# Kernel optimization log

Measured on AMD Instinct MI355X. Metric: run time of the kernel, lower is better.

The kernel has to match this reference:

```python
import jax, jax.numpy as jnp
import numpy as np

V = 20000   # token vocab (num_embeddings)
SC = 4000   # sub-char vocab (new_size of sub_char embedding)
D = 128     # embedding_dim
L = 15      # max nodes per decomposition tree (<= 8 leaves)
B, S = 32, 512


def _build_trees(rng):
    """Random binary decomposition trees in topological order (children < parent)."""
    node_ids = np.zeros((V, L), np.int32)
    left = np.full((V, L), -1, np.int32)
    right = np.full((V, L), -1, np.int32)
    last = np.zeros((V,), np.int32)
    for v in range(V):
        n_leaves = int(rng.integers(2, 9))
        stack, nodes = [], []
        leaves_left = n_leaves
        while leaves_left > 0 or len(stack) > 1:
            if leaves_left > 0 and (len(stack) < 2 or rng.random() < 0.5):
                nodes.append((-1, -1)); leaves_left -= 1
            else:
                r = stack.pop(); l = stack.pop()
                nodes.append((l, r))
            stack.append(len(nodes) - 1)
        n = len(nodes)
        for j, (l, r) in enumerate(nodes):
            left[v, j] = l; right[v, j] = r
        node_ids[v, :n] = rng.integers(0, SC, n)
        last[v] = n - 1
    return node_ids, left, right, last


def setup_inputs() -> dict:
    key = jax.random.key(0)
    k1, k2, k3, k4 = jax.random.split(key, 4)
    rng = np.random.default_rng(0)
    node_ids, left, right, last = _build_trees(rng)
    inp = {
        "input": jax.random.randint(k1, (B, S), 0, V, dtype=jnp.int32),
        "node_ids": jnp.asarray(node_ids),
        "left": jnp.asarray(left),
        "right": jnp.asarray(right),
        "last": jnp.asarray(last),
        "emb": jax.random.normal(k2, (SC, 5 * D), jnp.float32) * 0.1,   # sub_char weights
        "Wlh_w": jax.random.normal(k3, (D, 5 * D), jnp.float32) * 0.05,  # Linear(D,5D), x @ W
        "Wlh_b": jnp.zeros((5 * D,), jnp.float32),
        "Wrh_w": jax.random.normal(k4, (D, 5 * D), jnp.float32) * 0.05,
        "Wrh_b": jnp.zeros((5 * D,), jnp.float32),
    }
    return inp


def _tree_lstm(node_ids, left, right, last, emb, Wlh_w, Wlh_b, Wrh_w, Wrh_b):
    nV, nL = node_ids.shape
    gv = jnp.arange(nV)

    def step(carry, xs):
        h_all, c_all = carry                  # [V, L, D] each
        ids, l, r, j = xs                     # [V], [V], [V], scalar
        is_int = (l >= 0)[:, None]            # internal node mask; leaf has l==r==-1
        li, ri = jnp.maximum(l, 0), jnp.maximum(r, 0)
        hl, hr = h_all[gv, li], h_all[gv, ri]  # gather children states [V, D]
        cl, cr = c_all[gv, li], c_all[gv, ri]
        s = emb[ids]                           # [V, 5D]
        s_int = s + (hl @ Wlh_w + Wlh_b) + (hr @ Wrh_w + Wrh_b)
        s = jnp.where(is_int, s_int, s)
        ig, lfg, rfg, og, ug = jnp.split(s, 5, axis=1)
        c = jax.nn.sigmoid(ig) * jnp.tanh(ug)
        c = c + jnp.where(is_int, jax.nn.sigmoid(lfg) * cl + jax.nn.sigmoid(rfg) * cr, 0.0)
        h = jax.nn.sigmoid(og) * jnp.tanh(c)
        h_all = h_all.at[:, j].set(h)
        c_all = c_all.at[:, j].set(c)
        return (h_all, c_all), None

    init = (jnp.zeros((nV, nL, emb.shape[1] // 5), emb.dtype),
            jnp.zeros((nV, nL, emb.shape[1] // 5), emb.dtype))
    xs = (node_ids.T, left.T, right.T, jnp.arange(nL))
    (h_all, _), _ = jax.lax.scan(step, init, xs)
    return h_all[gv, last]                     # root h per vocab entry [V, D]


def reference(input, node_ids, left, right, last, emb, Wlh_w, Wlh_b, Wrh_w, Wrh_b):
    lut = _tree_lstm(node_ids, left, right, last, emb, Wlh_w, Wlh_b, Wrh_w, Wrh_b)  # [V, D]
    return lut[input]                          # [B, S, D]
```

## Files before the change

### kernel.cpp

```cpp
#include <hip/hip_runtime.h>
#include <hip/hip_fp16.h>
#include <math.h>

#define V    20000
#define SCV  4000
#define LL   15
#define OUTN (16384 * 128)

#define LEAF_BIT 0x40000000
#define REF_MASK 0x3FFFFFFF
#define ROOT_BIT 0x20000000
#define SLOT_MASK 0x1FFFFFFF
#define DUMMY_SLOT 89999

#define OFF_COUNTS 0
#define OFF_ROOT   128
#define OFF_LISTS  80384
#define OFF_LEAFC  5968384
#define OFF_LEAFHH 8016384
#define OFF_EMBT   9040384
#define OFF_WT     19280384
#define OFF_BIAS   19608064
#define OFF_HINT   19610624
#define OFF_CINT   65690624
#define OFF_HH     111770624
#define OFF_USED   134810624

__device__ __constant__ int d_listOff[8] = {0, 0, 80000, 120000, 160000, 180000, 200000, 220000};

#define MT 128

typedef _Float16 f16x8 __attribute__((ext_vector_type(8)));
typedef float    f32x4 __attribute__((ext_vector_type(4)));

__device__ __forceinline__ float sigm(float x) { return 1.0f / (1.0f + expf(-x)); }

__global__ void prep_kernel(const int* __restrict__ input,
                            const float* __restrict__ emb,
                            const float* __restrict__ Wl, const float* __restrict__ Wlb,
                            const float* __restrict__ Wr, const float* __restrict__ Wrb,
                            float* __restrict__ leafC, __half* __restrict__ leafHh,
                            __half* __restrict__ embT,
                            __half* __restrict__ WT, float* __restrict__ biasSum,
                            unsigned char* __restrict__ used) {
    __shared__ float T[64][65];
    int t = threadIdx.x, bid = blockIdx.x;
    for (int r = bid * 2 + (t >> 7); r < SCV; r += gridDim.x * 2) {
        int i = t & 127;
        const float* e = emb + r * 640;
        float c = sigm(e[i]) * tanhf(e[512 + i]);
        float h = sigm(e[384 + i]) * tanhf(c);
        leafC[r * 128 + i] = c;
        leafHh[r * 128 + i] = __float2half(h);
    }
    for (int idx = bid * 256 + t; idx < SCV * 128; idx += gridDim.x * 256) {
        int id = idx >> 7, dd = idx & 127;
        const float* e = emb + id * 640 + dd;
        __half v[8];
#pragma unroll
        for (int p = 0; p < 5; ++p) v[p] = __float2half(e[p * 128]);
        v[5] = __float2half(0.f); v[6] = v[5]; v[7] = v[5];
        *(uint4*)(embT + (size_t)idx * 8) = *(const uint4*)v;
    }
    for (int i = bid * 256 + t; i < 16384; i += gridDim.x * 256)
        used[input[i]] = 1;
    if (bid == 41)
        for (int i = t; i < 640; i += 256) biasSum[i] = Wlb[i] + Wrb[i];
    if (bid < 40) {
        int kb = (bid & 3) * 64, nb = (bid >> 2) * 64;
        int tx = t & 63, ty = t >> 6;
        for (int kk = ty; kk < 64; kk += 4) {
            int k = kb + kk;
            const float* Wsrc = (k < 128) ? (Wl + k * 640) : (Wr + (k - 128) * 640);
            T[kk][tx] = Wsrc[nb + tx];
        }
        __syncthreads();
        for (int nn = ty; nn < 64; nn += 4)
            WT[(nb + nn) * 256 + kb + tx] = __float2half(T[tx][nn]);
    }
}

__global__ void meta_kernel(const int* __restrict__ node_ids,
                            const int* __restrict__ left,
                            const int* __restrict__ right,
                            const int* __restrict__ last,
                            const unsigned char* __restrict__ used,
                            int* __restrict__ counts,
                            int* __restrict__ rootSlot,
                            int4* __restrict__ lists) {
    __shared__ int  sHei[MT][17];
    __shared__ int  sRef[MT][17];
    __shared__ int4 ebuf[MT][7];
    __shared__ int  ebin[MT][7];
    __shared__ int  locCnt[8];
    __shared__ int  basePos[8];
    __shared__ int  scanBuf[MT];
    __shared__ int  blockBase;

    int tid = threadIdx.x;
    if (tid < 8) locCnt[tid] = 0;
    __syncthreads();

    int v = blockIdx.x * MT + tid;
    int nInt = 0;
    if (v < V && used[v]) {
        int l15[LL], r15[LL], id15[LL];
#pragma unroll
        for (int j = 0; j < LL; ++j) {
            l15[j]  = left[v * LL + j];
            r15[j]  = right[v * LL + j];
            id15[j] = node_ids[v * LL + j];
        }
        int lastv = last[v];
#pragma unroll
        for (int j = 0; j < LL; ++j) {
            if (j <= lastv) {
                int l = l15[j];
                if (l < 0) {
                    sHei[tid][j] = 0;
                    sRef[tid][j] = LEAF_BIT | id15[j];
                } else {
                    int r = r15[j];
                    int hl = sHei[tid][l], hr = sHei[tid][r];
                    int hh = 1 + (hl > hr ? hl : hr);
                    sHei[tid][j] = hh;
                    int pos = atomicAdd(&locCnt[hh], 1);
                    int flag = (j == lastv) ? ROOT_BIT : 0;
                    ebuf[tid][nInt] = make_int4(nInt | flag, id15[j], sRef[tid][l], sRef[tid][r]);
                    ebin[tid][nInt] = (hh << 16) | pos;
                    sRef[tid][j] = nInt;
                    ++nInt;
                }
            }
        }
    }
    scanBuf[tid] = nInt;
    __syncthreads();
    for (int d = 1; d < MT; d <<= 1) {
        int val = (tid >= d) ? scanBuf[tid - d] : 0;
        __syncthreads();
        scanBuf[tid] += val;
        __syncthreads();
    }
    if (tid == 0) blockBase = atomicAdd(&counts[31], scanBuf[MT - 1]);
    if (tid < 8) {
        int c = locCnt[tid];
        basePos[tid] = c ? atomicAdd(&counts[tid], c) : 0;
    }
    __syncthreads();
    int treeBase = blockBase + scanBuf[tid] - nInt;
    if (v < V && nInt > 0) rootSlot[v] = treeBase + nInt - 1;
    for (int e = 0; e < nInt; ++e) {
        int4 E  = ebuf[tid][e];
        int md  = ebin[tid][e];
        int hh  = md >> 16, pos = md & 0xFFFF;
        E.x += treeBase;
        E.z = (E.z & LEAF_BIT) ? E.z : (E.z + treeBase);
        E.w = (E.w & LEAF_BIT) ? E.w : (E.w + treeBase);
        lists[d_listOff[hh] + basePos[hh] + pos] = E;
    }
}

__launch_bounds__(512, 4)
__global__ void round_mfma(const int4* __restrict__ list, const int* __restrict__ cntPtr,
                           const __half* __restrict__ embT, const __half* __restrict__ WT,
                           const float* __restrict__ biasSum,
                           const __half* __restrict__ leafHh, const float* __restrict__ leafC,
                           float* __restrict__ hInt, float* __restrict__ cInt,
                           __half* __restrict__ hH) {
    __shared__ __half Ah[32][264];
    __shared__ int4 meta[32];
    int cnt = *cntPtr;
    int nGroups = (cnt + 31) >> 5;
    int t = threadIdx.x;
    int lane = t & 63, wave = t >> 6;
    int ln15 = lane & 15, quad = lane >> 4;
    int d = 16 * wave + ln15;
    float bs[5];
#pragma unroll
    for (int p = 0; p < 5; ++p) bs[p] = biasSum[p * 128 + d];
    const __half* wbase = WT + d * 256 + quad * 8;

    for (int grp = blockIdx.x; grp < nGroups; grp += gridDim.x) {
        int base = grp * 32;
        int rows = cnt - base; if (rows > 32) rows = 32;
        if (t < 32) {
            int4 E;
            if (t < rows) E = list[base + t];
            else { E.x = DUMMY_SLOT; E.y = 0; E.z = LEAF_BIT; E.w = LEAF_BIT; }
            meta[t] = E;
        }
        __syncthreads();
#pragma unroll
        for (int it = 0; it < 2; ++it) {
            int idx = t + it * 512;
            int m = idx >> 5, q = idx & 31;
            int ref = (q < 16) ? meta[m].z : meta[m].w;
            const __half* hs = (ref & LEAF_BIT) ? leafHh : hH;
            uint4 v = *(const uint4*)(hs + (ref & REF_MASK) * 128 + (q & 15) * 8);
            *(uint4*)(&Ah[m][q * 8]) = v;
        }
        f32x4 acc[2][5];
#pragma unroll
        for (int c = 0; c < 2; ++c)
#pragma unroll
            for (int r = 0; r < 4; ++r) {
                int id = meta[c * 16 + quad * 4 + r].y;
                f16x8 ev = *(const f16x8*)((const void*)(embT + ((size_t)id * 128 + d) * 8));
#pragma unroll
                for (int p = 0; p < 5; ++p)
                    acc[c][p][r] = (float)ev[p] + bs[p];
            }
        __syncthreads();
#pragma unroll 2
        for (int kb = 0; kb < 8; ++kb) {
            f16x8 bf[5];
#pragma unroll
            for (int p = 0; p < 5; ++p)
                bf[p] = *(const f16x8*)((const void*)(wbase + p * 32768 + kb * 32));
            f16x8 af[2];
#pragma unroll
            for (int c = 0; c < 2; ++c)
                af[c] = *(const f16x8*)((const void*)&Ah[c * 16 + ln15][kb * 32 + quad * 8]);
#pragma unroll
            for (int p = 0; p < 5; ++p)
#pragma unroll
                for (int c = 0; c < 2; ++c)
                    acc[c][p] = __builtin_amdgcn_mfma_f32_16x16x32_f16(af[c], bf[p], acc[c][p], 0, 0, 0);
        }
#pragma unroll
        for (int c = 0; c < 2; ++c)
#pragma unroll
            for (int r = 0; r < 4; ++r) {
                int4 E = meta[c * 16 + quad * 4 + r];
                float ig = acc[c][0][r], lfg = acc[c][1][r], rfg = acc[c][2][r];
                float og = acc[c][3][r], ug = acc[c][4][r];
                float cl = ((E.z & LEAF_BIT) ? leafC : cInt)[(E.z & REF_MASK) * 128 + d];
                float cr = ((E.w & LEAF_BIT) ? leafC : cInt)[(E.w & REF_MASK) * 128 + d];
                float cc = sigm(ig) * tanhf(ug) + sigm(lfg) * cl + sigm(rfg) * cr;
                float hh2 = sigm(og) * tanhf(cc);
                int slot = E.x & SLOT_MASK;
                if (E.x & ROOT_BIT) {
                    hInt[slot * 128 + d] = hh2;
                } else {
                    cInt[slot * 128 + d] = cc;
                    hH[slot * 128 + d] = __float2half(hh2);
                }
            }
        __syncthreads();
    }
}

__global__ void gather_kernel(const int* __restrict__ input,
                              const int* __restrict__ rootSlot,
                              const float* __restrict__ hInt,
                              float4* __restrict__ out) {
    int idx = blockIdx.x * 256 + threadIdx.x;
    int token = input[idx >> 5];
    int d = idx & 31;
    out[idx] = ((const float4*)hInt)[rootSlot[token] * 32 + d];
}

extern "C" void kernel_launch(void* const* d_in, const int* in_sizes, int n_in,
                              void* d_out, int out_size, void* d_ws, size_t ws_size,
                              hipStream_t stream) {
    const int*   input    = (const int*)d_in[0];
    const int*   node_ids = (const int*)d_in[1];
    const int*   left     = (const int*)d_in[2];
    const int*   right    = (const int*)d_in[3];
    const int*   last     = (const int*)d_in[4];
    const float* emb      = (const float*)d_in[5];
    const float* Wl       = (const float*)d_in[6];
    const float* Wlb      = (const float*)d_in[7];
    const float* Wr       = (const float*)d_in[8];
    const float* Wrb      = (const float*)d_in[9];
    float* out = (float*)d_out;

    char* ws = (char*)d_ws;
    int*    counts   = (int*)(ws + OFF_COUNTS);
    int*    rootSlot = (int*)(ws + OFF_ROOT);
    int4*   lists    = (int4*)(ws + OFF_LISTS);
    float*  leafC    = (float*)(ws + OFF_LEAFC);
    __half* leafHh   = (__half*)(ws + OFF_LEAFHH);
    __half* embT     = (__half*)(ws + OFF_EMBT);
    __half* WT       = (__half*)(ws + OFF_WT);
    float*  biasSum  = (float*)(ws + OFF_BIAS);
    float*  hInt     = (float*)(ws + OFF_HINT);
    float*  cInt     = (float*)(ws + OFF_CINT);
    __half* hH       = (__half*)(ws + OFF_HH);
    unsigned char* usedp = (unsigned char*)(ws + OFF_USED);

    (void)hipMemsetAsync(counts, 0, 128, stream);
    (void)hipMemsetAsync(usedp, 0, V, stream);

    prep_kernel<<<1024, 256, 0, stream>>>(input, emb, Wl, Wlb, Wr, Wrb,
                                          leafC, leafHh, embT, WT, biasSum, usedp);
    meta_kernel<<<(V + MT - 1) / MT, MT, 0, stream>>>(node_ids, left, right, last, usedp,
                                                      counts, rootSlot, lists);

    static const int h_listOff[8] = {0, 0, 80000, 120000, 160000, 180000, 200000, 220000};
    static const int h_grid[8]    = {0, 1024, 512, 256, 128, 32, 16, 8};
    for (int h = 1; h <= 7; ++h) {
        round_mfma<<<h_grid[h], 512, 0, stream>>>(
            lists + h_listOff[h], counts + h,
            embT, WT, biasSum, leafHh, leafC, hInt, cInt, hH);
    }

    gather_kernel<<<OUTN / 4 / 256, 256, 0, stream>>>(input, rootSlot, hInt, (float4*)out);
}
```

Baseline: 326.3 us.

## Load MFMA A operands directly from global, shrink group to 16 rows

The per-round tree-LSTM kernel now processes 16 nodes per group instead of 32 and drops the shared-memory staging of child h vectors and metadata. Each lane reads its A fragment directly from global memory and loads its node metadata into registers, removing two block barriers per group. Grid sizes per height are raised to give the smaller groups more blocks. In exchange, each weight fragment is reused across half as many rows, so weight traffic per node doubles.

After: 502.1 us. +53.9%, slower.

```diff
diff --git a/kernel.cpp b/kernel.cpp
--- a/kernel.cpp
+++ b/kernel.cpp
@@ -168,10 +168,8 @@
                            const __half* __restrict__ leafHh, const float* __restrict__ leafC,
                            float* __restrict__ hInt, float* __restrict__ cInt,
                            __half* __restrict__ hH) {
-    __shared__ __half Ah[32][264];
-    __shared__ int4 meta[32];
     int cnt = *cntPtr;
-    int nGroups = (cnt + 31) >> 5;
+    int nGroups = (cnt + 15) >> 4;
     int t = threadIdx.x;
     int lane = t & 63, wave = t >> 6;
     int ln15 = lane & 15, quad = lane >> 4;
@@ -182,71 +180,53 @@
     const __half* wbase = WT + d * 256 + quad * 8;
 
     for (int grp = blockIdx.x; grp < nGroups; grp += gridDim.x) {
-        int base = grp * 32;
-        int rows = cnt - base; if (rows > 32) rows = 32;
-        if (t < 32) {
-            int4 E;
-            if (t < rows) E = list[base + t];
-            else { E.x = DUMMY_SLOT; E.y = 0; E.z = LEAF_BIT; E.w = LEAF_BIT; }
-            meta[t] = E;
-        }
-        __syncthreads();
-#pragma unroll
-        for (int it = 0; it < 2; ++it) {
-            int idx = t + it * 512;
-            int m = idx >> 5, q = idx & 31;
-            int ref = (q < 16) ? meta[m].z : meta[m].w;
-            const __half* hs = (ref & LEAF_BIT) ? leafHh : hH;
-            uint4 v = *(const uint4*)(hs + (ref & REF_MASK) * 128 + (q & 15) * 8);
-            *(uint4*)(&Ah[m][q * 8]) = v;
-        }
-        f32x4 acc[2][5];
-#pragma unroll
-        for (int c = 0; c < 2; ++c)
-#pragma unroll
-            for (int r = 0; r < 4; ++r) {
-                int id = meta[c * 16 + quad * 4 + r].y;
-                f16x8 ev = *(const f16x8*)((const void*)(embT + ((size_t)id * 128 + d) * 8));
-#pragma unroll
-                for (int p = 0; p < 5; ++p)
-                    acc[c][p][r] = (float)ev[p] + bs[p];
+        int base = grp * 16;
+        int rz = LEAF_BIT, rw = LEAF_BIT;
+        if (base + ln15 < cnt) { int4 E = list[base + ln15]; rz = E.z; rw = E.w; }
+        const __half* aPL = ((rz & LEAF_BIT) ? leafHh : hH) + (rz & REF_MASK) * 128;
+        const __half* aPR = ((rw & LEAF_BIT) ? leafHh : hH) + (rw & REF_MASK) * 128;
+        int4 Er[4];
+#pragma unroll
+        for (int r = 0; r < 4; ++r) {
+            int m = quad * 4 + r;
+            if (base + m < cnt) Er[r] = list[base + m];
+            else { Er[r].x = DUMMY_SLOT; Er[r].y = 0; Er[r].z = LEAF_BIT; Er[r].w = LEAF_BIT; }
+        }
+        f32x4 acc[5];
+#pragma unroll
+        for (int r = 0; r < 4; ++r) {
+            f16x8 ev = *(const f16x8*)((const void*)(embT + ((size_t)Er[r].y * 128 + d) * 8));
+#pragma unroll
+            for (int p = 0; p < 5; ++p)
+                acc[p][r] = (float)ev[p] + bs[p];
+        }
+#pragma unroll
+        for (int kb = 0; kb < 8; ++kb) {
+            const __half* aSrc = (kb < 4) ? aPL : aPR;
+            f16x8 af = *(const f16x8*)((const void*)(aSrc + (kb & 3) * 32 + quad * 8));
+#pragma unroll
+            for (int p = 0; p < 5; ++p) {
+                f16x8 bf = *(const f16x8*)((const void*)(wbase + p * 32768 + kb * 32));
+                acc[p] = __builtin_amdgcn_mfma_f32_16x16x32_f16(af, bf, acc[p], 0, 0, 0);
             }
-        __syncthreads();
-#pragma unroll 2
-        for (int kb = 0; kb < 8; ++kb) {
-            f16x8 bf[5];
-#pragma unroll
-            for (int p = 0; p < 5; ++p)
-                bf[p] = *(const f16x8*)((const void*)(wbase + p * 32768 + kb * 32));
-            f16x8 af[2];
-#pragma unroll
-            for (int c = 0; c < 2; ++c)
-                af[c] = *(const f16x8*)((const void*)&Ah[c * 16 + ln15][kb * 32 + quad * 8]);
-#pragma unroll
-            for (int p = 0; p < 5; ++p)
-#pragma unroll
-                for (int c = 0; c < 2; ++c)
-                    acc[c][p] = __builtin_amdgcn_mfma_f32_16x16x32_f16(af[c], bf[p], acc[c][p], 0, 0, 0);
-        }
-#pragma unroll
-        for (int c = 0; c < 2; ++c)
-#pragma unroll
-            for (int r = 0; r < 4; ++r) {
-                int4 E = meta[c * 16 + quad * 4 + r];
-                float ig = acc[c][0][r], lfg = acc[c][1][r], rfg = acc[c][2][r];
-                float og = acc[c][3][r], ug = acc[c][4][r];
-                float cl = ((E.z & LEAF_BIT) ? leafC : cInt)[(E.z & REF_MASK) * 128 + d];
-                float cr = ((E.w & LEAF_BIT) ? leafC : cInt)[(E.w & REF_MASK) * 128 + d];
-                float cc = sigm(ig) * tanhf(ug) + sigm(lfg) * cl + sigm(rfg) * cr;
-                float hh2 = sigm(og) * tanhf(cc);
-                int slot = E.x & SLOT_MASK;
-                if (E.x & ROOT_BIT) {
-                    hInt[slot * 128 + d] = hh2;
-                } else {
-                    cInt[slot * 128 + d] = cc;
-                    hH[slot * 128 + d] = __float2half(hh2);
-                }
+        }
+#pragma unroll
+        for (int r = 0; r < 4; ++r) {
+            int4 E = Er[r];
+            float ig = acc[0][r], lfg = acc[1][r], rfg = acc[2][r];
+            float og = acc[3][r], ug = acc[4][r];
+            float cl = ((E.z & LEAF_BIT) ? leafC : cInt)[(E.z & REF_MASK) * 128 + d];
+            float cr = ((E.w & LEAF_BIT) ? leafC : cInt)[(E.w & REF_MASK) * 128 + d];
+            float cc = sigm(ig) * tanhf(ug) + sigm(lfg) * cl + sigm(rfg) * cr;
+            float hh2 = sigm(og) * tanhf(cc);
+            int slot = E.x & SLOT_MASK;
+            if (E.x & ROOT_BIT) {
+                hInt[slot * 128 + d] = hh2;
+            } else {
+                cInt[slot * 128 + d] = cc;
+                hH[slot * 128 + d] = __float2half(hh2);
             }
+        }
         __syncthreads();
     }
 }
@@ -299,7 +279,7 @@
                                                       counts, rootSlot, lists);
 
     static const int h_listOff[8] = {0, 0, 80000, 120000, 160000, 180000, 200000, 220000};
-    static const int h_grid[8]    = {0, 1024, 512, 256, 128, 32, 16, 8};
+    static const int h_grid[8]    = {0, 1024, 768, 384, 192, 64, 32, 16};
     for (int h = 1; h <= 7; ++h) {
         round_mfma<<<h_grid[h], 512, 0, stream>>>(
             lists + h_listOff[h], counts + h,
```
